# Kernel tuning notes

Measured on AMD Instinct MI355X. Metric: run time of the kernel, lower is better.

Reference implementation:

```python
import jax, jax.numpy as jnp
import numpy as np

B, T, DIM = 2, 2048, 1024
HID = 4096
H, KVH, HD = 16, 4, 64
WIN = 512
NORM_EPS = 1e-5
QK_EPS = 1e-6
LS_INIT = 0.01


def setup_inputs() -> dict:
    key = jax.random.key(0)
    ks = jax.random.split(key, 12)
    s = lambda fan_in: 1.0 / np.sqrt(fan_in)
    return {
        "x": jax.random.normal(ks[0], (B, T, DIM), jnp.float32),
        # torch Linear weights are (out, in); y = x @ W.T
        "wq": jax.random.normal(ks[1], (H * HD, DIM), jnp.float32) * s(DIM),
        "wk": jax.random.normal(ks[2], (KVH * HD, DIM), jnp.float32) * s(DIM),
        "wv": jax.random.normal(ks[3], (KVH * HD, DIM), jnp.float32) * s(DIM),
        "wo": jax.random.normal(ks[4], (DIM, H * HD), jnp.float32) * s(H * HD),
        "w1": jax.random.normal(ks[5], (HID, DIM), jnp.float32) * s(DIM),
        "w2": jax.random.normal(ks[6], (DIM, HID), jnp.float32) * s(HID),
        "w3": jax.random.normal(ks[7], (HID, DIM), jnp.float32) * s(DIM),
        "q_norm_w": jnp.ones((HD,), jnp.float32),
        "k_norm_w": jnp.ones((HD,), jnp.float32),
        "attn_norm_w": jnp.ones((DIM,), jnp.float32),
        "ffn_norm_w": jnp.ones((DIM,), jnp.float32),
        "attn_scale": jnp.full((DIM,), LS_INIT, jnp.float32),
        "ffn_scale": jnp.full((DIM,), LS_INIT, jnp.float32),
    }


def _rmsnorm(x, w, eps):
    return x * jax.lax.rsqrt(jnp.mean(x * x, axis=-1, keepdims=True) + eps) * w


def _attention(x, wq, wk, wv, wo, q_norm_w, k_norm_w):
    b, t, _ = x.shape
    q = (x @ wq.T).reshape(b, t, H, HD)
    k = (x @ wk.T).reshape(b, t, KVH, HD)
    v = (x @ wv.T).reshape(b, t, KVH, HD)
    q = _rmsnorm(q, q_norm_w, QK_EPS)
    k = _rmsnorm(k, k_norm_w, QK_EPS)
    # GQA: repeat kv heads to H heads
    rep = H // KVH
    k = jnp.repeat(k, rep, axis=2)  # (b,t,H,HD)
    v = jnp.repeat(v, rep, axis=2)
    scale = 1.0 / np.sqrt(HD)
    scores = jnp.einsum("bqhd,bkhd->bhqk", q, k) * scale  # (b,H,t,t)
    row = jnp.arange(t)[:, None]
    col = jnp.arange(t)[None, :]
    mask = (row >= col) & (row - col < WIN)  # (t,t) bool
    scores = jnp.where(mask[None, None], scores, -jnp.inf)
    probs = jax.nn.softmax(scores, axis=-1)
    y = jnp.einsum("bhqk,bkhd->bqhd", probs, v).reshape(b, t, H * HD)
    return y @ wo.T


def reference(x, wq, wk, wv, wo, w1, w2, w3, q_norm_w, k_norm_w,
              attn_norm_w, ffn_norm_w, attn_scale, ffn_scale):
    r = _attention(_rmsnorm(x, attn_norm_w, NORM_EPS), wq, wk, wv, wo,
                   q_norm_w, k_norm_w)
    h = x + r * attn_scale
    hn = _rmsnorm(h, ffn_norm_w, NORM_EPS)
    ffn = (jax.nn.silu(hn @ w1.T) * (hn @ w3.T)) @ w2.T
    return h + ffn * ffn_scale
```

## Files before the change

### kernel.cpp

```cpp
#include <hip/hip_runtime.h>

typedef unsigned short u16;
typedef unsigned int u32;
typedef unsigned char u8;
typedef short bf16x8 __attribute__((ext_vector_type(8)));
typedef float f32x4 __attribute__((ext_vector_type(4)));
typedef float f32x16 __attribute__((ext_vector_type(16)));
typedef int i32x4 __attribute__((ext_vector_type(4)));
typedef int i32x8 __attribute__((ext_vector_type(8)));

#define AS1 __attribute__((address_space(1)))
#define AS3 __attribute__((address_space(3)))

#define B_ 2
#define T_ 2048
#define DIM_ 1024
#define HID_ 4096
#define H_ 16
#define KVH_ 4
#define HD_ 64
#define WIN_ 512

#define SCALE_A 0x7C7C7C7C
#define SCALE_B 0x79797979

__device__ __forceinline__ u16 f2bf(float f) {
    union { float f; u32 u; } v; v.f = f;
    u32 r = v.u + 0x7FFFu + ((v.u >> 16) & 1u);
    return (u16)(r >> 16);
}
__device__ __forceinline__ float bf2f(u32 u) {
    union { u32 u; float f; } v; v.u = u << 16;
    return v.f;
}
__device__ __forceinline__ float4 ld4bf(const u16* p) {
    uint2 u = *(const uint2*)p;
    float4 r;
    r.x = bf2f(u.x & 0xFFFFu); r.y = bf2f(u.x >> 16);
    r.z = bf2f(u.y & 0xFFFFu); r.w = bf2f(u.y >> 16);
    return r;
}
__device__ __forceinline__ void load_lds16(const void* g, void* l) {
    __builtin_amdgcn_global_load_lds((AS1 void*)(g), (AS3 void*)(l), 16, 0, 0);
}

__global__ __launch_bounds__(256) void mega_cvt(const float* __restrict__ wq,
                                                const float* __restrict__ wk,
                                                const float* __restrict__ wv,
                                                const float* __restrict__ wo,
                                                const float* __restrict__ w1,
                                                const float* __restrict__ w3,
                                                const float* __restrict__ w2,
                                                u16* __restrict__ wqkv,
                                                u16* __restrict__ wo_b,
                                                u8* __restrict__ w13_8,
                                                u8* __restrict__ w2_8) {
    int i = blockIdx.x * 256 + threadIdx.x;
    if (i < 655360) {
        const float* s; uint2* dbase; size_t didx;
        if (i < 262144)      { s = wq + (size_t)i * 4; dbase = (uint2*)wqkv; didx = i; }
        else if (i < 327680) { int f = i - 262144; s = wk + (size_t)f * 4; dbase = (uint2*)wqkv; didx = 262144 + f; }
        else if (i < 393216) { int f = i - 327680; s = wv + (size_t)f * 4; dbase = (uint2*)wqkv; didx = 327680 + f; }
        else                 { int f = i - 393216; s = wo + (size_t)f * 4; dbase = (uint2*)wo_b; didx = f; }
        float4 v = *(const float4*)s;
        u32 lo = (u32)f2bf(v.x) | ((u32)f2bf(v.y) << 16);
        u32 hi = (u32)f2bf(v.z) | ((u32)f2bf(v.w) << 16);
        dbase[didx] = make_uint2(lo, hi);
    } else {
        const float* s; u32* dbase; size_t didx;
        if (i < 1703936)      { int f = i - 655360;  int c = f >> 8; int n = (c >> 5) * 64 + (c & 31);
                                s = w1 + (size_t)f * 4; dbase = (u32*)w13_8; didx = (size_t)n * 256 + (f & 255); }
        else if (i < 2752512) { int f = i - 1703936; int c = f >> 8; int n = (c >> 5) * 64 + 32 + (c & 31);
                                s = w3 + (size_t)f * 4; dbase = (u32*)w13_8; didx = (size_t)n * 256 + (f & 255); }
        else                  { int f = i - 2752512; s = w2 + (size_t)f * 4; dbase = (u32*)w2_8; didx = f; }
        float4 v = *(const float4*)s;
        int p = __builtin_amdgcn_cvt_pk_fp8_f32(v.x * 64.f, v.y * 64.f, 0, false);
        p = __builtin_amdgcn_cvt_pk_fp8_f32(v.z * 64.f, v.w * 64.f, p, true);
        dbase[didx] = (u32)p;
    }
}

__global__ __launch_bounds__(256) void rmsnorm_kernel(const float* __restrict__ x,
                                                      const float* __restrict__ w,
                                                      u16* __restrict__ out, float eps) {
    int row = blockIdx.x, tid = threadIdx.x;
    const float4 v = ((const float4*)(x + (size_t)row * DIM_))[tid];
    float ss = v.x * v.x + v.y * v.y + v.z * v.z + v.w * v.w;
#pragma unroll
    for (int m = 1; m < 64; m <<= 1) ss += __shfl_xor(ss, m);
    __shared__ float part[4];
    if ((tid & 63) == 0) part[tid >> 6] = ss;
    __syncthreads();
    float tot = part[0] + part[1] + part[2] + part[3];
    float r = rsqrtf(tot * (1.0f / DIM_) + eps);
    const float4 wv = ((const float4*)w)[tid];
    u32 lo = (u32)f2bf(v.x * r * wv.x) | ((u32)f2bf(v.y * r * wv.y) << 16);
    u32 hi = (u32)f2bf(v.z * r * wv.z) | ((u32)f2bf(v.w * r * wv.w) << 16);
    ((uint2*)(out + (size_t)row * DIM_))[tid] = make_uint2(lo, hi);
}

__global__ __launch_bounds__(256) void fuse_attn_kernel(const float* __restrict__ x,
                                                        const u16* __restrict__ p,
                                                        const float* __restrict__ ascale,
                                                        const float* __restrict__ fnw,
                                                        float* __restrict__ h,
                                                        u8* __restrict__ xn8) {
    int row = blockIdx.x, tid = threadIdx.x;
    const float4 xv = ((const float4*)(x + (size_t)row * DIM_))[tid];
    float4 a0 = ld4bf(p + (size_t)row * DIM_ + tid * 4);
    float4 a1 = ld4bf(p + 4194304 + (size_t)row * DIM_ + tid * 4);
    const float4 sc = ((const float4*)ascale)[tid];
    float4 hv;
    hv.x = xv.x + (a0.x + a1.x) * sc.x;
    hv.y = xv.y + (a0.y + a1.y) * sc.y;
    hv.z = xv.z + (a0.z + a1.z) * sc.z;
    hv.w = xv.w + (a0.w + a1.w) * sc.w;
    ((float4*)(h + (size_t)row * DIM_))[tid] = hv;
    float ss = hv.x * hv.x + hv.y * hv.y + hv.z * hv.z + hv.w * hv.w;
#pragma unroll
    for (int m = 1; m < 64; m <<= 1) ss += __shfl_xor(ss, m);
    __shared__ float part[4];
    if ((tid & 63) == 0) part[tid >> 6] = ss;
    __syncthreads();
    float tot = part[0] + part[1] + part[2] + part[3];
    float r = rsqrtf(tot * (1.0f / DIM_) + 1e-5f) * 8.0f;
    const float4 wv = ((const float4*)fnw)[tid];
    int pk = __builtin_amdgcn_cvt_pk_fp8_f32(hv.x * r * wv.x, hv.y * r * wv.y, 0, false);
    pk = __builtin_amdgcn_cvt_pk_fp8_f32(hv.z * r * wv.z, hv.w * r * wv.w, pk, true);
    ((u32*)xn8)[(size_t)row * 256 + tid] = (u32)pk;
}

__global__ __launch_bounds__(256) void fuse_ffn_kernel(const float* __restrict__ h,
                                                       const u16* __restrict__ p,
                                                       const float* __restrict__ fscale,
                                                       float* __restrict__ out) {
    int row = blockIdx.x, tid = threadIdx.x;
    const float4 hv = ((const float4*)(h + (size_t)row * DIM_))[tid];
    size_t off = (size_t)row * DIM_ + tid * 4;
    float4 a0 = ld4bf(p + off);
    float4 a1 = ld4bf(p + 4194304 + off);
    float4 a2 = ld4bf(p + 8388608 + off);
    float4 a3 = ld4bf(p + 12582912 + off);
    const float4 sc = ((const float4*)fscale)[tid];
    float4 o;
    o.x = hv.x + (a0.x + a1.x + a2.x + a3.x) * sc.x;
    o.y = hv.y + (a0.y + a1.y + a2.y + a3.y) * sc.y;
    o.z = hv.z + (a0.z + a1.z + a2.z + a3.z) * sc.z;
    o.w = hv.w + (a0.w + a1.w + a2.w + a3.w) * sc.w;
    ((float4*)(out + (size_t)row * DIM_))[tid] = o;
}

__global__ __launch_bounds__(256) void qkv_post_kernel(const u16* __restrict__ qkv,
                                                       const float* __restrict__ qw,
                                                       const float* __restrict__ kw,
                                                       u16* __restrict__ Qb,
                                                       u16* __restrict__ Kb,
                                                       u16* __restrict__ Vb) {
    int bt = blockIdx.x;
    int b = bt >> 11, t = bt & (T_ - 1);
    int wave = threadIdx.x >> 6, lane = threadIdx.x & 63;
    const u16* row0 = qkv + (size_t)bt * 1536;
    const u16* row1 = row0 + 6291456;
    float qwl = qw[lane], kwl = kw[lane];
#pragma unroll
    for (int i = 0; i < 4; i++) {
        int h = wave * 4 + i;
        float v = bf2f(row0[h * 64 + lane]) + bf2f(row1[h * 64 + lane]);
        float ss = v * v;
#pragma unroll
        for (int m = 1; m < 64; m <<= 1) ss += __shfl_xor(ss, m);
        float r = rsqrtf(ss * (1.0f / 64.0f) + 1e-6f);
        Qb[(((size_t)(b * H_ + h)) * T_ + t) * HD_ + lane] = f2bf(v * r * qwl);
    }
    {
        float v = bf2f(row0[1024 + wave * 64 + lane]) + bf2f(row1[1024 + wave * 64 + lane]);
        float ss = v * v;
#pragma unroll
        for (int m = 1; m < 64; m <<= 1) ss += __shfl_xor(ss, m);
        float r = rsqrtf(ss * (1.0f / 64.0f) + 1e-6f);
        Kb[(((size_t)(b * KVH_ + wave)) * T_ + t) * HD_ + lane] = f2bf(v * r * kwl);
        float vv = bf2f(row0[1280 + wave * 64 + lane]) + bf2f(row1[1280 + wave * 64 + lane]);
        Vb[(((size_t)(b * KVH_ + wave)) * T_ + t) * HD_ + lane] = f2bf(vv);
    }
}

__global__ __launch_bounds__(256) void flash_kernel(const u16* __restrict__ Qb,
                                                    const u16* __restrict__ Kb,
                                                    const u16* __restrict__ Vb,
                                                    u16* __restrict__ Ob) {
    const int b = blockIdx.z, h = blockIdx.y, qt = blockIdx.x;
    const int q0 = qt * 64;
    const int tid = threadIdx.x, wave = tid >> 6, lane = tid & 63;
    const int m = lane & 15, quad = lane >> 4;
    const int kvh = h >> 2;

    __shared__ __align__(16) u16 Ks[32 * 64];
    __shared__ __align__(16) u16 Vts[64 * 32];
    __shared__ __align__(16) u16 Ps[4][16 * 32];

    const u16* Qp = Qb + ((size_t)(b * H_ + h) * T_) * HD_;
    const u16* Kp = Kb + ((size_t)(b * KVH_ + kvh) * T_) * HD_;
    const u16* Vp = Vb + ((size_t)(b * KVH_ + kvh) * T_) * HD_;

    const int qrow = q0 + wave * 16 + m;
    bf16x8 qa0 = *(const bf16x8*)(Qp + (size_t)qrow * 64 + quad * 8);
    bf16x8 qa1 = *(const bf16x8*)(Qp + (size_t)qrow * 64 + 32 + quad * 8);

    f32x4 o0 = {0.f, 0.f, 0.f, 0.f}, o1 = {0.f, 0.f, 0.f, 0.f};
    f32x4 o2 = {0.f, 0.f, 0.f, 0.f}, o3 = {0.f, 0.f, 0.f, 0.f};
    float mrun[4] = {-INFINITY, -INFINITY, -INFINITY, -INFINITY};
    float lrun[4] = {0.f, 0.f, 0.f, 0.f};

    const int klo = (q0 - (WIN_ - 1) > 0) ? (q0 - (WIN_ - 1)) : 0;
    const int kt0 = klo >> 5, kt1 = (q0 + 63) >> 5;
    const int qlo_w = q0 + wave * 16, qhi_w = qlo_w + 15;

    for (int kt = kt0; kt <= kt1; ++kt) {
        const int kbase = kt << 5;
        __syncthreads();
        {
            int flat = tid * 8;
            int kr = flat >> 6, d = flat & 63;
            *(bf16x8*)&Ks[flat] = *(const bf16x8*)(Kp + (size_t)(kbase + kr) * 64 + d);
            bf16x8 vv = *(const bf16x8*)(Vp + (size_t)(kbase + kr) * 64 + d);
#pragma unroll
            for (int jj = 0; jj < 8; jj++) Vts[(d + jj) * 32 + kr] = (u16)vv[jj];
        }
        __syncthreads();
        bool active = (kbase <= qhi_w) && (kbase + 31 >= qlo_w - (WIN_ - 1));
        if (active) {
            f32x4 s0 = {0.f, 0.f, 0.f, 0.f}, s1 = {0.f, 0.f, 0.f, 0.f};
            bf16x8 k00 = *(const bf16x8*)&Ks[m * 64 + quad * 8];
            bf16x8 k01 = *(const bf16x8*)&Ks[m * 64 + 32 + quad * 8];
            bf16x8 k10 = *(const bf16x8*)&Ks[(m + 16) * 64 + quad * 8];
            bf16x8 k11 = *(const bf16x8*)&Ks[(m + 16) * 64 + 32 + quad * 8];
            s0 = __builtin_amdgcn_mfma_f32_16x16x32_bf16(qa0, k00, s0, 0, 0, 0);
            s0 = __builtin_amdgcn_mfma_f32_16x16x32_bf16(qa1, k01, s0, 0, 0, 0);
            s1 = __builtin_amdgcn_mfma_f32_16x16x32_bf16(qa0, k10, s1, 0, 0, 0);
            s1 = __builtin_amdgcn_mfma_f32_16x16x32_bf16(qa1, k11, s1, 0, 0, 0);
#pragma unroll
            for (int r = 0; r < 4; r++) {
                int qg = q0 + wave * 16 + quad * 4 + r;
                int kg0 = kbase + m, kg1 = kbase + 16 + m;
                float v0 = (kg0 <= qg && qg - kg0 < WIN_) ? s0[r] * 0.125f : -INFINITY;
                float v1 = (kg1 <= qg && qg - kg1 < WIN_) ? s1[r] * 0.125f : -INFINITY;
                float rmax = fmaxf(v0, v1);
                rmax = fmaxf(rmax, __shfl_xor(rmax, 1));
                rmax = fmaxf(rmax, __shfl_xor(rmax, 2));
                rmax = fmaxf(rmax, __shfl_xor(rmax, 4));
                rmax = fmaxf(rmax, __shfl_xor(rmax, 8));
                float mnew = fmaxf(mrun[r], rmax);
                float alpha, p0, p1;
                if (mnew == -INFINITY) { alpha = 1.f; p0 = 0.f; p1 = 0.f; }
                else {
                    alpha = __expf(mrun[r] - mnew);
                    p0 = __expf(v0 - mnew);
                    p1 = __expf(v1 - mnew);
                }
                float psum = p0 + p1;
                psum += __shfl_xor(psum, 1);
                psum += __shfl_xor(psum, 2);
                psum += __shfl_xor(psum, 4);
                psum += __shfl_xor(psum, 8);
                lrun[r] = lrun[r] * alpha + psum;
                mrun[r] = mnew;
                o0[r] *= alpha; o1[r] *= alpha; o2[r] *= alpha; o3[r] *= alpha;
                Ps[wave][(quad * 4 + r) * 32 + m] = f2bf(p0);
                Ps[wave][(quad * 4 + r) * 32 + 16 + m] = f2bf(p1);
            }
            bf16x8 pa = *(const bf16x8*)&Ps[wave][m * 32 + quad * 8];
            bf16x8 vb0 = *(const bf16x8*)&Vts[(0 + m) * 32 + quad * 8];
            bf16x8 vb1 = *(const bf16x8*)&Vts[(16 + m) * 32 + quad * 8];
            bf16x8 vb2 = *(const bf16x8*)&Vts[(32 + m) * 32 + quad * 8];
            bf16x8 vb3 = *(const bf16x8*)&Vts[(48 + m) * 32 + quad * 8];
            o0 = __builtin_amdgcn_mfma_f32_16x16x32_bf16(pa, vb0, o0, 0, 0, 0);
            o1 = __builtin_amdgcn_mfma_f32_16x16x32_bf16(pa, vb1, o1, 0, 0, 0);
            o2 = __builtin_amdgcn_mfma_f32_16x16x32_bf16(pa, vb2, o2, 0, 0, 0);
            o3 = __builtin_amdgcn_mfma_f32_16x16x32_bf16(pa, vb3, o3, 0, 0, 0);
        }
    }
#pragma unroll
    for (int r = 0; r < 4; r++) {
        int qg = q0 + wave * 16 + quad * 4 + r;
        float inv = 1.0f / lrun[r];
        size_t base = ((size_t)(b * T_ + qg)) * (H_ * HD_) + h * HD_;
        Ob[base + 0 + m] = f2bf(o0[r] * inv);
        Ob[base + 16 + m] = f2bf(o1[r] * inv);
        Ob[base + 32 + m] = f2bf(o2[r] * inv);
        Ob[base + 48 + m] = f2bf(o3[r] * inv);
    }
}

__global__ __launch_bounds__(256) void gemm_bt(const u16* __restrict__ A,
                                               const u16* __restrict__ Bt,
                                               u16* __restrict__ Cb,
                                               int M, int N, int K, int KS) {
    __shared__ __align__(16) u16 As[2][4096];
    __shared__ __align__(16) u16 Bs[2][4096];
    const int tid = threadIdx.x, wave = tid >> 6, lane = tid & 63;
    const int m = lane & 15, quad = lane >> 4;
    const int m0 = blockIdx.y * 128, n0 = blockIdx.x * 128;
    const int wm = (wave >> 1) * 64, wn = (wave & 1) * 64;
    const int kb = blockIdx.z * KS;
    const int nIter = KS >> 5;
    const int slot = wave * 2;
    const int flat0 = slot * 512 + lane * 8;
    const int row0_ = flat0 >> 5, col0 = flat0 & 31;
    const int flat1 = (slot + 1) * 512 + lane * 8;
    const int row1_ = flat1 >> 5, col1 = flat1 & 31;

    f32x4 acc[4][4] = {};

    load_lds16(A + (size_t)(m0 + row0_) * K + kb + col0, &As[0][slot * 512]);
    load_lds16(Bt + (size_t)(n0 + row0_) * K + kb + col0, &Bs[0][slot * 512]);
    load_lds16(A + (size_t)(m0 + row1_) * K + kb + col1, &As[0][(slot + 1) * 512]);
    load_lds16(Bt + (size_t)(n0 + row1_) * K + kb + col1, &Bs[0][(slot + 1) * 512]);

    for (int it = 0; it < nIter; ++it) {
        __syncthreads();
        const int cur = it & 1;
        if (it + 1 < nIter) {
            const int nb = 1 - cur;
            const int k0 = kb + (it + 1) * 32;
            load_lds16(A + (size_t)(m0 + row0_) * K + k0 + col0, &As[nb][slot * 512]);
            load_lds16(Bt + (size_t)(n0 + row0_) * K + k0 + col0, &Bs[nb][slot * 512]);
            load_lds16(A + (size_t)(m0 + row1_) * K + k0 + col1, &As[nb][(slot + 1) * 512]);
            load_lds16(Bt + (size_t)(n0 + row1_) * K + k0 + col1, &Bs[nb][(slot + 1) * 512]);
        }
        bf16x8 af[4], bfr[4];
#pragma unroll
        for (int i = 0; i < 4; i++) af[i] = *(const bf16x8*)&As[cur][(wm + i * 16 + m) * 32 + quad * 8];
#pragma unroll
        for (int j = 0; j < 4; j++) bfr[j] = *(const bf16x8*)&Bs[cur][(wn + j * 16 + m) * 32 + quad * 8];
#pragma unroll
        for (int i = 0; i < 4; i++)
#pragma unroll
            for (int j = 0; j < 4; j++)
                acc[i][j] = __builtin_amdgcn_mfma_f32_16x16x32_bf16(af[i], bfr[j], acc[i][j], 0, 0, 0);
    }

    u16* Cz = Cb + (size_t)blockIdx.z * M * N;
#pragma unroll
    for (int i = 0; i < 4; i++) {
        int rowb = m0 + wm + i * 16 + quad * 4;
#pragma unroll
        for (int j = 0; j < 4; j++) {
            int col = n0 + wn + j * 16 + m;
#pragma unroll
            for (int r = 0; r < 4; r++)
                Cz[(size_t)(rowb + r) * N + col] = f2bf(acc[i][j][r]);
        }
    }
}

#define MFMA8(a, b, c) __builtin_amdgcn_mfma_scale_f32_32x32x64_f8f6f4(a, b, c, 0, 0, 0, SCALE_A, 0, SCALE_B)
#define WAITBAR(N) asm volatile("s_waitcnt vmcnt(" #N ")\n\ts_barrier" ::: "memory")
#define PHASE_MFMA(I0, I1)                           \
    __builtin_amdgcn_s_setprio(1);                   \
    acc[I0][0] = MFMA8(a0, bf0, acc[I0][0]);         \
    acc[I0][1] = MFMA8(a0, bf1, acc[I0][1]);         \
    acc[I1][0] = MFMA8(a1, bf0, acc[I1][0]);         \
    acc[I1][1] = MFMA8(a1, bf1, acc[I1][1]);         \
    __builtin_amdgcn_s_setprio(0);

template <int MODE>
__global__ __launch_bounds__(512) void gemm_fp8(const u8* __restrict__ A,
                                                const u8* __restrict__ Bt,
                                                u16* __restrict__ Cb,
                                                u8* __restrict__ C8,
                                                int M, int N, int K, int KS) {
    __shared__ __align__(16) u8 As[2][32768];
    __shared__ __align__(16) u8 Bs[2][32768];
    const int tid = threadIdx.x, wave = tid >> 6, lane = tid & 63;
    const int l31 = lane & 31, lh = lane >> 5;
    const int m0 = blockIdx.y * 256, n0 = blockIdx.x * 256;
    const int wm = (wave >> 2) * 128, wn = (wave & 3) * 64;
    const int kb = blockIdx.z * KS;
    const int KT = KS >> 7;

    const int srow = ((wave & 3) << 6) + lane;
    const u8* Asrc = A + (size_t)m0 * K + (size_t)srow * K;
    const u8* Bsrc = Bt + (size_t)n0 * K + (size_t)srow * K;
    const int wv2 = wave >> 2;
    const int ldsW = (wave & 3) << 10;

    auto STAGE = [&](const u8* src, int kk, int ks, u8* lds) {
#pragma unroll
        for (int q = 0; q < 2; q++) {
            const int ch = ks * 4 + wv2 + 2 * q;
            load_lds16(src + kk + ch * 16, lds + (ch << 12) + ldsW);
        }
    };
    auto FRAG = [&](const u8* t, int ks, int row) -> i32x8 {
        const int c0 = ks * 4 + (lh << 1);
        union { i32x4 h[2]; i32x8 v; } u;
        u.h[0] = *(const i32x4*)(t + ((c0 << 8) + row) * 16);
        u.h[1] = *(const i32x4*)(t + (((c0 + 1) << 8) + row) * 16);
        return u.v;
    };

    f32x16 acc[4][2] = {};

    STAGE(Asrc, kb, 0, As[0]);
    STAGE(Bsrc, kb, 0, Bs[0]);
    STAGE(Asrc, kb, 1, As[0]);
    STAGE(Bsrc, kb, 1, Bs[0]);

    for (int kt = 0; kt < KT - 1; ++kt) {
        const int cur = kt & 1, nb = cur ^ 1;
        const u8* Ac = As[cur];
        const u8* Bc = Bs[cur];
        const int kn = kb + (kt + 1) * 128;
        i32x8 bf0, bf1, a0, a1;
        STAGE(Asrc, kn, 0, As[nb]);
        WAITBAR(6);
        bf0 = FRAG(Bc, 0, wn + l31);
        bf1 = FRAG(Bc, 0, wn + 32 + l31);
        a0 = FRAG(Ac, 0, wm + l31);
        a1 = FRAG(Ac, 0, wm + 32 + l31);
        PHASE_MFMA(0, 1)
        STAGE(Bsrc, kn, 0, Bs[nb]);
        a0 = FRAG(Ac, 0, wm + 64 + l31);
        a1 = FRAG(Ac, 0, wm + 96 + l31);
        PHASE_MFMA(2, 3)
        STAGE(Asrc, kn, 1, As[nb]);
        WAITBAR(6);
        bf0 = FRAG(Bc, 1, wn + l31);
        bf1 = FRAG(Bc, 1, wn + 32 + l31);
        a0 = FRAG(Ac, 1, wm + l31);
        a1 = FRAG(Ac, 1, wm + 32 + l31);
        PHASE_MFMA(0, 1)
        STAGE(Bsrc, kn, 1, Bs[nb]);
        a0 = FRAG(Ac, 1, wm + 64 + l31);
        a1 = FRAG(Ac, 1, wm + 96 + l31);
        PHASE_MFMA(2, 3)
    }
    {
        const int cur = (KT - 1) & 1;
        const u8* Ac = As[cur];
        const u8* Bc = Bs[cur];
        i32x8 bf0, bf1, a0, a1;
        WAITBAR(4);
        bf0 = FRAG(Bc, 0, wn + l31);
        bf1 = FRAG(Bc, 0, wn + 32 + l31);
        a0 = FRAG(Ac, 0, wm + l31);
        a1 = FRAG(Ac, 0, wm + 32 + l31);
        PHASE_MFMA(0, 1)
        a0 = FRAG(Ac, 0, wm + 64 + l31);
        a1 = FRAG(Ac, 0, wm + 96 + l31);
        PHASE_MFMA(2, 3)
        WAITBAR(0);
        bf0 = FRAG(Bc, 1, wn + l31);
        bf1 = FRAG(Bc, 1, wn + 32 + l31);
        a0 = FRAG(Ac, 1, wm + l31);
        a1 = FRAG(Ac, 1, wm + 32 + l31);
        PHASE_MFMA(0, 1)
        a0 = FRAG(Ac, 1, wm + 64 + l31);
        a1 = FRAG(Ac, 1, wm + 96 + l31);
        PHASE_MFMA(2, 3)
    }

    if (MODE == 0) {
        u16* Cz = Cb + (size_t)blockIdx.z * M * N;
#pragma unroll
        for (int i = 0; i < 4; i++)
#pragma unroll
            for (int j = 0; j < 2; j++) {
                int col = n0 + wn + j * 32 + l31;
#pragma unroll
                for (int reg = 0; reg < 16; reg++) {
                    int row = m0 + wm + i * 32 + (reg & 3) + 8 * (reg >> 2) + 4 * lh;
                    Cz[(size_t)row * N + col] = f2bf(acc[i][j][reg]);
                }
            }
    } else {
        int c = (n0 >> 1) + (wn >> 1) + l31;
#pragma unroll
        for (int i = 0; i < 4; i++)
#pragma unroll
            for (int reg = 0; reg < 16; reg++) {
                int row = m0 + wm + i * 32 + (reg & 3) + 8 * (reg >> 2) + 4 * lh;
                float g1 = acc[i][0][reg], g3 = acc[i][1][reg];
                float res = (g1 / (1.f + __expf(-g1))) * g3 * 8.0f;
                int p = __builtin_amdgcn_cvt_pk_fp8_f32(res, res, 0, false);
                C8[(size_t)row * (N >> 1) + c] = (u8)(p & 0xFF);
            }
    }
}

extern "C" void kernel_launch(void* const* d_in, const int* in_sizes, int n_in,
                              void* d_out, int out_size, void* d_ws, size_t ws_size,
                              hipStream_t stream) {
    const float* x = (const float*)d_in[0];
    const float* wq = (const float*)d_in[1];
    const float* wk = (const float*)d_in[2];
    const float* wv = (const float*)d_in[3];
    const float* wo = (const float*)d_in[4];
    const float* w1 = (const float*)d_in[5];
    const float* w2 = (const float*)d_in[6];
    const float* w3 = (const float*)d_in[7];
    const float* qnw = (const float*)d_in[8];
    const float* knw = (const float*)d_in[9];
    const float* anw = (const float*)d_in[10];
    const float* fnw = (const float*)d_in[11];
    const float* ascale = (const float*)d_in[12];
    const float* fscale = (const float*)d_in[13];
    float* out = (float*)d_out;

    char* ws = (char*)d_ws;
    u16* wqkv_bf = (u16*)(ws + 0);
    u16* wo_bf = (u16*)(ws + 3145728);
    u8* w13_8 = (u8*)(ws + 5242880);
    u8* w2_8 = (u8*)(ws + 13631488);
    u16* xn_bf = (u16*)(ws + 17825792);
    u8* xn8 = (u8*)(ws + 26214400);
    float* h_f = (float*)(ws + 30408704);
    char* P = ws + 47185920;
    u16* qkv_part = (u16*)(P + 0);
    u16* Qb = (u16*)(P + 25165824);
    u16* Kb = (u16*)(P + 33554432);
    u16* Vb = (u16*)(P + 35651584);
    u16* att_bf = (u16*)(P + 37748736);
    u16* wo_part = (u16*)(P + 0);
    u8* gsw8 = (u8*)(P + 16777216);
    u16* w2_part = (u16*)(P + 33554432);

    mega_cvt<<<14848, 256, 0, stream>>>(wq, wk, wv, wo, w1, w3, w2,
                                        wqkv_bf, wo_bf, w13_8, w2_8);
    rmsnorm_kernel<<<4096, 256, 0, stream>>>(x, anw, xn_bf, 1e-5f);
    gemm_bt<<<dim3(12, 32, 2), 256, 0, stream>>>(xn_bf, wqkv_bf, qkv_part,
                                                 4096, 1536, 1024, 512);
    qkv_post_kernel<<<4096, 256, 0, stream>>>(qkv_part, qnw, knw, Qb, Kb, Vb);
    flash_kernel<<<dim3(32, 16, 2), 256, 0, stream>>>(Qb, Kb, Vb, att_bf);
    gemm_bt<<<dim3(8, 32, 2), 256, 0, stream>>>(att_bf, wo_bf, wo_part,
                                                4096, 1024, 1024, 512);
    fuse_attn_kernel<<<4096, 256, 0, stream>>>(x, wo_part, ascale, fnw, h_f, xn8);
    gemm_fp8<1><<<dim3(32, 16, 1), 512, 0, stream>>>(xn8, w13_8, nullptr, gsw8,
                                                     4096, 8192, 1024, 1024);
    gemm_fp8<0><<<dim3(4, 16, 4), 512, 0, stream>>>(gsw8, w2_8, w2_part, nullptr,
                                                    4096, 1024, 4096, 1024);
    fuse_ffn_kernel<<<4096, 256, 0, stream>>>(h_f, w2_part, fscale, out);
}
```

Baseline: 355.7 us.

## Drop LDS staging in flash attention; load K/V directly with pre-transposed V

Adds a kernel that transposes V to (d, t) layout once, so the flash kernel can load V operands for the PV MFMA straight from global memory. K fragments are register-prefetched one tile ahead, which removes the per-tile LDS staging and both block-wide barriers. Each wave now iterates only over its own 16-row key range, applies the mask only on edge tiles, and pads the P scratch to avoid bank conflicts. It trades LDS sharing of K/V across the four waves for redundant global/L2 loads, and adds an extra launch.

```diff
diff --git a/kernel.cpp b/kernel.cpp
--- a/kernel.cpp
+++ b/kernel.cpp
@@ -184,9 +184,32 @@
     }
 }
 
+__global__ __launch_bounds__(256) void vtrans_kernel(const u16* __restrict__ Vb,
+                                                     u16* __restrict__ Vt) {
+    const int bk = blockIdx.x >> 5;
+    const int t0 = (blockIdx.x & 31) * 64;
+    const int tid = threadIdx.x;
+    __shared__ __align__(16) u16 tile[64][64];
+    const u16* src = Vb + ((size_t)bk * T_ + t0) * HD_;
+#pragma unroll
+    for (int i = 0; i < 2; i++) {
+        int g = tid + i * 256;
+        int r = g >> 3, c8 = g & 7;
+        *(bf16x8*)&tile[r][c8 * 8] = *(const bf16x8*)(src + (size_t)r * HD_ + c8 * 8);
+    }
+    __syncthreads();
+    const int d = tid >> 2, ts = (tid & 3) * 16;
+    u16 buf[16];
+#pragma unroll
+    for (int j = 0; j < 16; j++) buf[j] = tile[ts + j][d];
+    u16* dst = Vt + (size_t)bk * HD_ * T_ + (size_t)d * T_ + t0 + ts;
+    *(bf16x8*)(dst) = *(const bf16x8*)&buf[0];
+    *(bf16x8*)(dst + 8) = *(const bf16x8*)&buf[8];
+}
+
 __global__ __launch_bounds__(256) void flash_kernel(const u16* __restrict__ Qb,
                                                     const u16* __restrict__ Kb,
-                                                    const u16* __restrict__ Vb,
+                                                    const u16* __restrict__ Vt,
                                                     u16* __restrict__ Ob) {
     const int b = blockIdx.z, h = blockIdx.y, qt = blockIdx.x;
     const int q0 = qt * 64;
@@ -194,90 +217,88 @@
     const int m = lane & 15, quad = lane >> 4;
     const int kvh = h >> 2;
 
-    __shared__ __align__(16) u16 Ks[32 * 64];
-    __shared__ __align__(16) u16 Vts[64 * 32];
-    __shared__ __align__(16) u16 Ps[4][16 * 32];
+    __shared__ __align__(16) u16 Ps[4][16 * 40];
 
     const u16* Qp = Qb + ((size_t)(b * H_ + h) * T_) * HD_;
     const u16* Kp = Kb + ((size_t)(b * KVH_ + kvh) * T_) * HD_;
-    const u16* Vp = Vb + ((size_t)(b * KVH_ + kvh) * T_) * HD_;
-
-    const int qrow = q0 + wave * 16 + m;
+    const u16* Vp = Vt + ((size_t)(b * KVH_ + kvh) * HD_) * T_;
+
+    const int qlo = q0 + wave * 16;
+    const int qrow = qlo + m;
     bf16x8 qa0 = *(const bf16x8*)(Qp + (size_t)qrow * 64 + quad * 8);
     bf16x8 qa1 = *(const bf16x8*)(Qp + (size_t)qrow * 64 + 32 + quad * 8);
 
     f32x4 o0 = {0.f, 0.f, 0.f, 0.f}, o1 = {0.f, 0.f, 0.f, 0.f};
     f32x4 o2 = {0.f, 0.f, 0.f, 0.f}, o3 = {0.f, 0.f, 0.f, 0.f};
-    float mrun[4] = {-INFINITY, -INFINITY, -INFINITY, -INFINITY};
+    float mrun[4] = {-1e30f, -1e30f, -1e30f, -1e30f};
     float lrun[4] = {0.f, 0.f, 0.f, 0.f};
 
-    const int klo = (q0 - (WIN_ - 1) > 0) ? (q0 - (WIN_ - 1)) : 0;
-    const int kt0 = klo >> 5, kt1 = (q0 + 63) >> 5;
-    const int qlo_w = q0 + wave * 16, qhi_w = qlo_w + 15;
+    const int klo = (qlo - (WIN_ - 1) > 0) ? (qlo - (WIN_ - 1)) : 0;
+    const int kt0 = klo >> 5, kt1 = (qlo + 15) >> 5;
+
+    const u16* kp0 = Kp + (size_t)(kt0 * 32 + m) * 64 + quad * 8;
+    bf16x8 k00 = *(const bf16x8*)(kp0);
+    bf16x8 k01 = *(const bf16x8*)(kp0 + 32);
+    bf16x8 k10 = *(const bf16x8*)(kp0 + 16 * 64);
+    bf16x8 k11 = *(const bf16x8*)(kp0 + 16 * 64 + 32);
 
     for (int kt = kt0; kt <= kt1; ++kt) {
         const int kbase = kt << 5;
-        __syncthreads();
-        {
-            int flat = tid * 8;
-            int kr = flat >> 6, d = flat & 63;
-            *(bf16x8*)&Ks[flat] = *(const bf16x8*)(Kp + (size_t)(kbase + kr) * 64 + d);
-            bf16x8 vv = *(const bf16x8*)(Vp + (size_t)(kbase + kr) * 64 + d);
-#pragma unroll
-            for (int jj = 0; jj < 8; jj++) Vts[(d + jj) * 32 + kr] = (u16)vv[jj];
+        f32x4 s0 = {0.f, 0.f, 0.f, 0.f}, s1 = {0.f, 0.f, 0.f, 0.f};
+        s0 = __builtin_amdgcn_mfma_f32_16x16x32_bf16(qa0, k00, s0, 0, 0, 0);
+        s0 = __builtin_amdgcn_mfma_f32_16x16x32_bf16(qa1, k01, s0, 0, 0, 0);
+        s1 = __builtin_amdgcn_mfma_f32_16x16x32_bf16(qa0, k10, s1, 0, 0, 0);
+        s1 = __builtin_amdgcn_mfma_f32_16x16x32_bf16(qa1, k11, s1, 0, 0, 0);
+        const u16* vp = Vp + (size_t)m * T_ + kbase + quad * 8;
+        bf16x8 vb0 = *(const bf16x8*)(vp);
+        bf16x8 vb1 = *(const bf16x8*)(vp + 16 * T_);
+        bf16x8 vb2 = *(const bf16x8*)(vp + 32 * T_);
+        bf16x8 vb3 = *(const bf16x8*)(vp + 48 * T_);
+        if (kt < kt1) {
+            const u16* kp = Kp + (size_t)(kbase + 32 + m) * 64 + quad * 8;
+            k00 = *(const bf16x8*)(kp);
+            k01 = *(const bf16x8*)(kp + 32);
+            k10 = *(const bf16x8*)(kp + 16 * 64);
+            k11 = *(const bf16x8*)(kp + 16 * 64 + 32);
         }
-        __syncthreads();
-        bool active = (kbase <= qhi_w) && (kbase + 31 >= qlo_w - (WIN_ - 1));
-        if (active) {
-            f32x4 s0 = {0.f, 0.f, 0.f, 0.f}, s1 = {0.f, 0.f, 0.f, 0.f};
-            bf16x8 k00 = *(const bf16x8*)&Ks[m * 64 + quad * 8];
-            bf16x8 k01 = *(const bf16x8*)&Ks[m * 64 + 32 + quad * 8];
-            bf16x8 k10 = *(const bf16x8*)&Ks[(m + 16) * 64 + quad * 8];
-            bf16x8 k11 = *(const bf16x8*)&Ks[(m + 16) * 64 + 32 + quad * 8];
-            s0 = __builtin_amdgcn_mfma_f32_16x16x32_bf16(qa0, k00, s0, 0, 0, 0);
-            s0 = __builtin_amdgcn_mfma_f32_16x16x32_bf16(qa1, k01, s0, 0, 0, 0);
-            s1 = __builtin_amdgcn_mfma_f32_16x16x32_bf16(qa0, k10, s1, 0, 0, 0);
-            s1 = __builtin_amdgcn_mfma_f32_16x16x32_bf16(qa1, k11, s1, 0, 0, 0);
-#pragma unroll
-            for (int r = 0; r < 4; r++) {
-                int qg = q0 + wave * 16 + quad * 4 + r;
+        const bool full = (kbase + 31 <= qlo) && (kbase >= qlo - 496);
+#pragma unroll
+        for (int r = 0; r < 4; r++) {
+            float v0, v1;
+            if (full) {
+                v0 = s0[r] * 0.125f;
+                v1 = s1[r] * 0.125f;
+            } else {
+                int qg = qlo + quad * 4 + r;
                 int kg0 = kbase + m, kg1 = kbase + 16 + m;
-                float v0 = (kg0 <= qg && qg - kg0 < WIN_) ? s0[r] * 0.125f : -INFINITY;
-                float v1 = (kg1 <= qg && qg - kg1 < WIN_) ? s1[r] * 0.125f : -INFINITY;
-                float rmax = fmaxf(v0, v1);
-                rmax = fmaxf(rmax, __shfl_xor(rmax, 1));
-                rmax = fmaxf(rmax, __shfl_xor(rmax, 2));
-                rmax = fmaxf(rmax, __shfl_xor(rmax, 4));
-                rmax = fmaxf(rmax, __shfl_xor(rmax, 8));
-                float mnew = fmaxf(mrun[r], rmax);
-                float alpha, p0, p1;
-                if (mnew == -INFINITY) { alpha = 1.f; p0 = 0.f; p1 = 0.f; }
-                else {
-                    alpha = __expf(mrun[r] - mnew);
-                    p0 = __expf(v0 - mnew);
-                    p1 = __expf(v1 - mnew);
-                }
-                float psum = p0 + p1;
-                psum += __shfl_xor(psum, 1);
-                psum += __shfl_xor(psum, 2);
-                psum += __shfl_xor(psum, 4);
-                psum += __shfl_xor(psum, 8);
-                lrun[r] = lrun[r] * alpha + psum;
-                mrun[r] = mnew;
-                o0[r] *= alpha; o1[r] *= alpha; o2[r] *= alpha; o3[r] *= alpha;
-                Ps[wave][(quad * 4 + r) * 32 + m] = f2bf(p0);
-                Ps[wave][(quad * 4 + r) * 32 + 16 + m] = f2bf(p1);
+                v0 = (kg0 <= qg && qg - kg0 < WIN_) ? s0[r] * 0.125f : -INFINITY;
+                v1 = (kg1 <= qg && qg - kg1 < WIN_) ? s1[r] * 0.125f : -INFINITY;
             }
-            bf16x8 pa = *(const bf16x8*)&Ps[wave][m * 32 + quad * 8];
-            bf16x8 vb0 = *(const bf16x8*)&Vts[(0 + m) * 32 + quad * 8];
-            bf16x8 vb1 = *(const bf16x8*)&Vts[(16 + m) * 32 + quad * 8];
-            bf16x8 vb2 = *(const bf16x8*)&Vts[(32 + m) * 32 + quad * 8];
-            bf16x8 vb3 = *(const bf16x8*)&Vts[(48 + m) * 32 + quad * 8];
-            o0 = __builtin_amdgcn_mfma_f32_16x16x32_bf16(pa, vb0, o0, 0, 0, 0);
-            o1 = __builtin_amdgcn_mfma_f32_16x16x32_bf16(pa, vb1, o1, 0, 0, 0);
-            o2 = __builtin_amdgcn_mfma_f32_16x16x32_bf16(pa, vb2, o2, 0, 0, 0);
-            o3 = __builtin_amdgcn_mfma_f32_16x16x32_bf16(pa, vb3, o3, 0, 0, 0);
+            float rmax = fmaxf(v0, v1);
+            rmax = fmaxf(rmax, __shfl_xor(rmax, 1));
+            rmax = fmaxf(rmax, __shfl_xor(rmax, 2));
+            rmax = fmaxf(rmax, __shfl_xor(rmax, 4));
+            rmax = fmaxf(rmax, __shfl_xor(rmax, 8));
+            float mnew = fmaxf(mrun[r], rmax);
+            float alpha = __expf(mrun[r] - mnew);
+            float p0 = __expf(v0 - mnew);
+            float p1 = __expf(v1 - mnew);
+            float psum = p0 + p1;
+            psum += __shfl_xor(psum, 1);
+            psum += __shfl_xor(psum, 2);
+            psum += __shfl_xor(psum, 4);
+            psum += __shfl_xor(psum, 8);
+            lrun[r] = lrun[r] * alpha + psum;
+            mrun[r] = mnew;
+            o0[r] *= alpha; o1[r] *= alpha; o2[r] *= alpha; o3[r] *= alpha;
+            Ps[wave][(quad * 4 + r) * 40 + m] = f2bf(p0);
+            Ps[wave][(quad * 4 + r) * 40 + 16 + m] = f2bf(p1);
         }
+        bf16x8 pa = *(const bf16x8*)&Ps[wave][m * 40 + quad * 8];
+        o0 = __builtin_amdgcn_mfma_f32_16x16x32_bf16(pa, vb0, o0, 0, 0, 0);
+        o1 = __builtin_amdgcn_mfma_f32_16x16x32_bf16(pa, vb1, o1, 0, 0, 0);
+        o2 = __builtin_amdgcn_mfma_f32_16x16x32_bf16(pa, vb2, o2, 0, 0, 0);
+        o3 = __builtin_amdgcn_mfma_f32_16x16x32_bf16(pa, vb3, o3, 0, 0, 0);
     }
 #pragma unroll
     for (int r = 0; r < 4; r++) {
@@ -521,6 +542,7 @@
     u16* Kb = (u16*)(P + 33554432);
     u16* Vb = (u16*)(P + 35651584);
     u16* att_bf = (u16*)(P + 37748736);
+    u16* Vt = (u16*)(P + 46137344);
     u16* wo_part = (u16*)(P + 0);
     u8* gsw8 = (u8*)(P + 16777216);
     u16* w2_part = (u16*)(P + 33554432);
@@ -531,7 +553,8 @@
     gemm_bt<<<dim3(12, 32, 2), 256, 0, stream>>>(xn_bf, wqkv_bf, qkv_part,
                                                  4096, 1536, 1024, 512);
     qkv_post_kernel<<<4096, 256, 0, stream>>>(qkv_part, qnw, knw, Qb, Kb, Vb);
-    flash_kernel<<<dim3(32, 16, 2), 256, 0, stream>>>(Qb, Kb, Vb, att_bf);
+    vtrans_kernel<<<256, 256, 0, stream>>>(Vb, Vt);
+    flash_kernel<<<dim3(32, 16, 2), 256, 0, stream>>>(Qb, Kb, Vt, att_bf);
     gemm_bt<<<dim3(8, 32, 2), 256, 0, stream>>>(att_bf, wo_bf, wo_part,
                                                 4096, 1024, 1024, 512);
     fuse_attn_kernel<<<4096, 256, 0, stream>>>(x, wo_part, ascale, fnw, h_f, xn8);
```

New measurement: 355.8 us. About the same (+0.0%).
